# Kernel tuning notes

Measured on AMD Instinct MI355X. Metric: run time of the kernel, lower is better.

The kernel has to match this reference:

```python
import jax, jax.numpy as jnp
import numpy as np

ENC_DIM = 256
DEC_DIM = 256
INT_DIM = 256


def setup_inputs() -> dict:
    key = jax.random.key(0)
    k1, k2, k3, k4, k5 = jax.random.split(key, 5)
    B, T = 64, 2048
    encoder_states = jax.random.normal(k1, (B, T, ENC_DIM), dtype=jnp.float32)
    decoder_state = jax.random.normal(k2, (B, DEC_DIM), dtype=jnp.float32)
    s1 = 1.0 / np.sqrt(ENC_DIM)
    s2 = 1.0 / np.sqrt(DEC_DIM)
    s3 = 1.0 / np.sqrt(INT_DIM)
    w1 = jax.random.uniform(k3, (INT_DIM, ENC_DIM), jnp.float32, -s1, s1)
    w2 = jax.random.uniform(k4, (INT_DIM, DEC_DIM), jnp.float32, -s2, s2)
    v = jax.random.uniform(k5, (1, INT_DIM), jnp.float32, -s3, s3)
    return {"encoder_states": encoder_states, "decoder_state": decoder_state,
            "w1": w1, "w2": w2, "v": v}


def reference(encoder_states, decoder_state, w1, w2, v):
    # scores: v @ tanh(W1 e_t + W2 d) for all t at once
    enc_proj = jnp.einsum('bte,ie->bti', encoder_states, w1)      # [B,T,I]
    dec_proj = jnp.einsum('bd,id->bi', decoder_state, w2)          # [B,I]
    scores = jnp.einsum('bti,oi->bt', jnp.tanh(enc_proj + dec_proj[:, None, :]), v)  # [B,T]
    attention_probs = jax.nn.softmax(scores, axis=1)[:, :, None]   # [B,T,1]
    final_context_vec = jnp.sum(attention_probs * encoder_states, axis=1)  # [B,E]
    return final_context_vec, attention_probs
```

## Files before the change

kernel.cpp:

```cpp
#include <hip/hip_runtime.h>
#include <hip/hip_bf16.h>
#include <math.h>

#define Bq 64
#define Tq 2048
#define Eq 256
#define Dq 256
#define Iq 256

using short8  = __attribute__((ext_vector_type(8))) short;
using floatx4 = __attribute__((ext_vector_type(4))) float;

__device__ __forceinline__ float fast_tanh(float x) {
    float e = __expf(2.0f * x);
    return fmaf(-2.0f, __builtin_amdgcn_rcpf(e + 1.0f), 1.0f);
}

__device__ __forceinline__ ushort f2bf(float x) {
    union { __hip_bfloat16 h; ushort u; } c;
    c.h = __float2bfloat16(x);
    return c.u;
}

__global__ __launch_bounds__(256) void prep_kernel(
    const float* __restrict__ w1, ushort* __restrict__ w1sw,
    const float* __restrict__ dec, const float* __restrict__ w2,
    float* __restrict__ dproj)
{
    if (blockIdx.x < 32) {
        const int kc = blockIdx.x;
        const int i  = threadIdx.x;
        const float* src = w1 + i * Eq + kc * 8;
        float4 f0 = *(const float4*)src;
        float4 f1 = *(const float4*)(src + 4);
        ushort u[8] = { f2bf(f0.x), f2bf(f0.y), f2bf(f0.z), f2bf(f0.w),
                        f2bf(f1.x), f2bf(f1.y), f2bf(f1.z), f2bf(f1.w) };
        *(short8*)&w1sw[(kc * 256 + i) * 8] = *(short8*)u;
    } else {
        const int b = blockIdx.x - 32;
        const int i = threadIdx.x;
        __shared__ float dls[Dq];
        dls[i] = dec[b * Dq + i];
        __syncthreads();
        const float* w2r = w2 + i * Dq;
        float acc = 0.f;
        #pragma unroll 8
        for (int d = 0; d < Dq; d += 4) {
            float4 wv = *(const float4*)&w2r[d];
            float4 dv = *(const float4*)&dls[d];
            acc += wv.x * dv.x + wv.y * dv.y + wv.z * dv.z + wv.w * dv.w;
        }
        dproj[b * Iq + i] = acc;
    }
}

__global__ __launch_bounds__(256, 3) void scores_ctx_kernel(
    const float*  __restrict__ enc,
    const ushort* __restrict__ w1sw,
    const float*  __restrict__ v,
    const float*  __restrict__ dproj,
    float* __restrict__ escore,
    float* __restrict__ ctxp,
    float* __restrict__ denomp)
{
    const int b   = blockIdx.y;
    const int bx  = blockIdx.x;
    const int t0  = bx * 64;
    const int tid = threadIdx.x;
    const int w   = tid >> 6;
    const int l   = tid & 63;
    const int l15 = l & 15;
    const int lq  = l >> 4;

    __shared__ alignas(16) ushort As[2][64 * 72];
    __shared__ float swred[4 * 64];
    __shared__ float redf[4 * 256];

    float vv[4], dd[4];
    #pragma unroll
    for (int ni = 0; ni < 4; ++ni) {
        const int i = w * 64 + ni * 16 + l15;
        vv[ni] = v[i];
        dd[ni] = dproj[b * Iq + i];
    }

    floatx4 acc[4][4];
    #pragma unroll
    for (int mi = 0; mi < 4; ++mi)
        #pragma unroll
        for (int ni = 0; ni < 4; ++ni)
            acc[mi][ni] = (floatx4)0.f;

    const float* encB = enc + ((size_t)b * Tq + t0) * Eq;
    const int srow = tid >> 4;
    const int sc4  = (tid & 15) * 4;

    #define LOADC(kt, st)                                                     \
        _Pragma("unroll")                                                     \
        for (int r = 0; r < 4; ++r)                                           \
            st[r] = *(const float4*)&encB[(srow + 16 * r) * Eq + (kt) * 64 + sc4];
    #define CVTW(st, buf)                                                     \
        _Pragma("unroll")                                                     \
        for (int r = 0; r < 4; ++r) {                                         \
            ushort4 u;                                                        \
            u.x = f2bf(st[r].x); u.y = f2bf(st[r].y);                         \
            u.z = f2bf(st[r].z); u.w = f2bf(st[r].w);                         \
            *(ushort4*)&As[buf][(srow + 16 * r) * 72 + sc4] = u;              \
        }
    #define BARRIER()                                                         \
        asm volatile("s_waitcnt lgkmcnt(0)" ::: "memory");                    \
        __builtin_amdgcn_s_barrier();                                         \
        __builtin_amdgcn_sched_barrier(0);

    const ushort* vb = w1sw + (w * 64 + l15) * 8 + lq * 2048;

    #define KSTEP(k, cur, LOADNEXT, CVTPREV)                                  \
    {                                                                         \
        short8 bfv[2][4];                                                     \
        _Pragma("unroll")                                                     \
        for (int ks = 0; ks < 2; ++ks)                                        \
            _Pragma("unroll")                                                 \
            for (int ni = 0; ni < 4; ++ni)                                    \
                bfv[ks][ni] = *(const short8*)(vb + ((k) * 8 + ks * 4) * 2048 \
                                               + ni * 128);                   \
        LOADNEXT                                                              \
        _Pragma("unroll")                                                     \
        for (int ks = 0; ks < 2; ++ks) {                                      \
            const int kloc = ks * 32 + lq * 8;                                \
            short8 af[4];                                                     \
            _Pragma("unroll")                                                 \
            for (int mi = 0; mi < 4; ++mi)                                    \
                af[mi] = *(const short8*)&As[cur][(mi * 16 + l15) * 72 + kloc];\
            __builtin_amdgcn_s_setprio(1);                                    \
            _Pragma("unroll")                                                 \
            for (int mi = 0; mi < 4; ++mi)                                    \
                _Pragma("unroll")                                             \
                for (int ni = 0; ni < 4; ++ni)                                \
                    acc[mi][ni] = __builtin_amdgcn_mfma_f32_16x16x32_bf16(    \
                        af[mi], bfv[ks][ni], acc[mi][ni], 0, 0, 0);           \
            __builtin_amdgcn_s_setprio(0);                                    \
        }                                                                     \
        CVTPREV                                                               \
    }

    float4 s0[4], s1[4];
    LOADC(0, s0);
    LOADC(1, s1);
    CVTW(s0, 0);
    BARRIER();

    KSTEP(0, 0, LOADC(2, s0);, CVTW(s1, 1); BARRIER();)
    KSTEP(1, 1, LOADC(3, s1);, CVTW(s0, 0); BARRIER();)
    KSTEP(2, 0, ;,             CVTW(s1, 1); BARRIER();)
    KSTEP(3, 1, ;,             ;)

    #undef KSTEP
    #undef LOADC
    #undef CVTW

    float part[4][4];
    #pragma unroll
    for (int mi = 0; mi < 4; ++mi)
        #pragma unroll
        for (int r = 0; r < 4; ++r) part[mi][r] = 0.f;

    #pragma unroll
    for (int ni = 0; ni < 4; ++ni) {
        const float vi = vv[ni];
        const float dp = dd[ni];
        #pragma unroll
        for (int mi = 0; mi < 4; ++mi)
            #pragma unroll
            for (int r = 0; r < 4; ++r)
                part[mi][r] += vi * fast_tanh(acc[mi][ni][r] + dp);
    }

    #pragma unroll
    for (int mi = 0; mi < 4; ++mi)
        #pragma unroll
        for (int r = 0; r < 4; ++r) {
            float x = part[mi][r];
            x += __shfl_xor(x, 1); x += __shfl_xor(x, 2);
            x += __shfl_xor(x, 4); x += __shfl_xor(x, 8);
            part[mi][r] = x;
        }
    if (l15 == 0) {
        #pragma unroll
        for (int mi = 0; mi < 4; ++mi)
            #pragma unroll
            for (int r = 0; r < 4; ++r)
                swred[w * 64 + mi * 16 + lq * 4 + r] = part[mi][r];
    }
    __syncthreads();

    float s = swred[l] + swred[64 + l] + swred[128 + l] + swred[192 + l];
    const float es = __expf(s);
    if (w == 0) {
        escore[(size_t)b * Tq + t0 + l] = es;
        float tot = es;
        tot += __shfl_xor(tot, 1);  tot += __shfl_xor(tot, 2);
        tot += __shfl_xor(tot, 4);  tot += __shfl_xor(tot, 8);
        tot += __shfl_xor(tot, 16); tot += __shfl_xor(tot, 32);
        if (l == 0) denomp[bx * Bq + b] = tot;
    }

    const int el = l * 4;
    float4 a = {0.f, 0.f, 0.f, 0.f};
    #pragma unroll 8
    for (int tt = 0; tt < 16; ++tt) {
        const int t = w * 16 + tt;
        const float pt = __shfl(es, t);
        float4 ev = *(const float4*)&encB[t * Eq + el];
        a.x += pt * ev.x; a.y += pt * ev.y; a.z += pt * ev.z; a.w += pt * ev.w;
    }
    *(float4*)&redf[w * 256 + el] = a;
    __syncthreads();
    if (w == 0) {
        float4 a0 = *(const float4*)&redf[0 * 256 + el];
        float4 a1 = *(const float4*)&redf[1 * 256 + el];
        float4 a2 = *(const float4*)&redf[2 * 256 + el];
        float4 a3 = *(const float4*)&redf[3 * 256 + el];
        float4 o;
        o.x = a0.x + a1.x + a2.x + a3.x;
        o.y = a0.y + a1.y + a2.y + a3.y;
        o.z = a0.z + a1.z + a2.z + a3.z;
        o.w = a0.w + a1.w + a2.w + a3.w;
        *(float4*)&ctxp[((size_t)bx * Bq + b) * Eq + el] = o;
    }
}

__global__ __launch_bounds__(256) void finalize_kernel(
    const float* __restrict__ ctxp, const float* __restrict__ denomp,
    float* __restrict__ probs, float* __restrict__ ctx)
{
    const int b   = blockIdx.x;
    const int tid = threadIdx.x;

    float d = denomp[(tid & 31) * Bq + b];
    d += __shfl_xor(d, 1);  d += __shfl_xor(d, 2);  d += __shfl_xor(d, 4);
    d += __shfl_xor(d, 8);  d += __shfl_xor(d, 16);
    const float inv = 1.0f / d;

    float* prow = probs + (size_t)b * Tq + tid * 8;
    float4 p0 = *(const float4*)(prow + 0);
    float4 p1 = *(const float4*)(prow + 4);
    p0.x *= inv; p0.y *= inv; p0.z *= inv; p0.w *= inv;
    p1.x *= inv; p1.y *= inv; p1.z *= inv; p1.w *= inv;
    *(float4*)(prow + 0) = p0;
    *(float4*)(prow + 4) = p1;

    float s = 0.f;
    #pragma unroll 8
    for (int c = 0; c < 32; ++c)
        s += ctxp[((size_t)c * Bq + b) * Eq + tid];
    ctx[b * Eq + tid] = s * inv;
}

extern "C" void kernel_launch(void* const* d_in, const int* in_sizes, int n_in,
                              void* d_out, int out_size, void* d_ws, size_t ws_size,
                              hipStream_t stream) {
    const float* enc = (const float*)d_in[0];
    const float* dec = (const float*)d_in[1];
    const float* w1  = (const float*)d_in[2];
    const float* w2  = (const float*)d_in[3];
    const float* v   = (const float*)d_in[4];

    float* out   = (float*)d_out;
    float* ctx   = out;
    float* probs = out + Bq * Eq;

    char* ws = (char*)d_ws;
    float*  ctxp   = (float*)ws;
    float*  denomp = (float*)(ws + (32*Bq*Eq)*4);
    float*  dproj  = (float*)(ws + (32*Bq*Eq)*4 + 32*Bq*4);
    ushort* w1sw   = (ushort*)(ws + (32*Bq*Eq)*4 + 32*Bq*4 + Bq*Iq*4);

    prep_kernel<<<dim3(96), dim3(256), 0, stream>>>(w1, w1sw, dec, w2, dproj);
    scores_ctx_kernel<<<dim3(Tq / 64, Bq), dim3(256), 0, stream>>>(
        enc, w1sw, v, dproj, probs, ctxp, denomp);
    finalize_kernel<<<dim3(Bq), dim3(256), 0, stream>>>(ctxp, denomp, probs, ctx);
}
```

Before: 218.3 us.

## Process two T-tiles per block and prefetch next tile's loads during the first epilogue

Each block now handles two consecutive 64-row time tiles instead of one, halving the grid. The first k-chunks of the second tile are loaded from global memory during the last MFMA steps of the first tile, so that load latency overlaps the first tile's tanh/softmax/context epilogue. This amortizes per-block setup (v, dproj loads) and hides the pipeline fill. In exchange the grid has fewer blocks (16x64), which may reduce occupancy and tail balance, and registers holding the prefetched tile stay live across the epilogue.

```diff
diff --git a/kernel.cpp b/kernel.cpp
--- a/kernel.cpp
+++ b/kernel.cpp
@@ -54,6 +54,91 @@
     }
 }
 
+__device__ __forceinline__ void tile_epilogue(
+    floatx4 (&acc)[4][4], const float (&vv)[4], const float (&dd)[4],
+    float* swred, float* redf, const float* eb,
+    float* __restrict__ escore, float* __restrict__ ctxp,
+    float* __restrict__ denomp,
+    int b, int bxx, int w, int l, int l15, int lq)
+{
+    float part[4][4];
+    #pragma unroll
+    for (int mi = 0; mi < 4; ++mi)
+        #pragma unroll
+        for (int r = 0; r < 4; ++r) part[mi][r] = 0.f;
+
+    #pragma unroll
+    for (int ni = 0; ni < 4; ++ni) {
+        const float vi = vv[ni];
+        const float dp = dd[ni];
+        #pragma unroll
+        for (int mi = 0; mi < 4; ++mi)
+            #pragma unroll
+            for (int r = 0; r < 4; ++r)
+                part[mi][r] += vi * fast_tanh(acc[mi][ni][r] + dp);
+    }
+
+    #pragma unroll
+    for (int mi = 0; mi < 4; ++mi)
+        #pragma unroll
+        for (int r = 0; r < 4; ++r) {
+            float x = part[mi][r];
+            x += __shfl_xor(x, 1); x += __shfl_xor(x, 2);
+            x += __shfl_xor(x, 4); x += __shfl_xor(x, 8);
+            part[mi][r] = x;
+        }
+    if (l15 == 0) {
+        #pragma unroll
+        for (int mi = 0; mi < 4; ++mi)
+            #pragma unroll
+            for (int r = 0; r < 4; ++r)
+                swred[w * 64 + mi * 16 + lq * 4 + r] = part[mi][r];
+    }
+    asm volatile("s_waitcnt lgkmcnt(0)" ::: "memory");
+    __builtin_amdgcn_s_barrier();
+    __builtin_amdgcn_sched_barrier(0);
+
+    float s = swred[l] + swred[64 + l] + swred[128 + l] + swred[192 + l];
+    const float es = __expf(s);
+    if (w == 0) {
+        escore[(size_t)b * Tq + bxx * 64 + l] = es;
+        float tot = es;
+        tot += __shfl_xor(tot, 1);  tot += __shfl_xor(tot, 2);
+        tot += __shfl_xor(tot, 4);  tot += __shfl_xor(tot, 8);
+        tot += __shfl_xor(tot, 16); tot += __shfl_xor(tot, 32);
+        if (l == 0) denomp[bxx * Bq + b] = tot;
+    }
+
+    const int el = l * 4;
+    float4 a = {0.f, 0.f, 0.f, 0.f};
+    #pragma unroll 8
+    for (int tt = 0; tt < 16; ++tt) {
+        const int t = w * 16 + tt;
+        const float pt = __shfl(es, t);
+        float4 ev = *(const float4*)&eb[t * Eq + el];
+        a.x += pt * ev.x; a.y += pt * ev.y; a.z += pt * ev.z; a.w += pt * ev.w;
+    }
+    *(float4*)&redf[w * 256 + el] = a;
+    asm volatile("s_waitcnt lgkmcnt(0)" ::: "memory");
+    __builtin_amdgcn_s_barrier();
+    __builtin_amdgcn_sched_barrier(0);
+    if (w == 0) {
+        float4 a0 = *(const float4*)&redf[0 * 256 + el];
+        float4 a1 = *(const float4*)&redf[1 * 256 + el];
+        float4 a2 = *(const float4*)&redf[2 * 256 + el];
+        float4 a3 = *(const float4*)&redf[3 * 256 + el];
+        float4 o;
+        o.x = a0.x + a1.x + a2.x + a3.x;
+        o.y = a0.y + a1.y + a2.y + a3.y;
+        o.z = a0.z + a1.z + a2.z + a3.z;
+        o.w = a0.w + a1.w + a2.w + a3.w;
+        *(float4*)&ctxp[((size_t)bxx * Bq + b) * Eq + el] = o;
+    }
+    asm volatile("s_waitcnt lgkmcnt(0)" ::: "memory");
+    __builtin_amdgcn_s_barrier();
+    __builtin_amdgcn_sched_barrier(0);
+}
+
 __global__ __launch_bounds__(256, 3) void scores_ctx_kernel(
     const float*  __restrict__ enc,
     const ushort* __restrict__ w1sw,
@@ -64,8 +149,7 @@
     float* __restrict__ denomp)
 {
     const int b   = blockIdx.y;
-    const int bx  = blockIdx.x;
-    const int t0  = bx * 64;
+    const int bx0 = blockIdx.x * 2;
     const int tid = threadIdx.x;
     const int w   = tid >> 6;
     const int l   = tid & 63;
@@ -85,20 +169,16 @@
     }
 
     floatx4 acc[4][4];
-    #pragma unroll
-    for (int mi = 0; mi < 4; ++mi)
-        #pragma unroll
-        for (int ni = 0; ni < 4; ++ni)
-            acc[mi][ni] = (floatx4)0.f;
-
-    const float* encB = enc + ((size_t)b * Tq + t0) * Eq;
+
+    const float* encT0 = enc + ((size_t)b * Tq + bx0 * 64) * Eq;
+    const float* encT1 = encT0 + (size_t)64 * Eq;
     const int srow = tid >> 4;
     const int sc4  = (tid & 15) * 4;
 
-    #define LOADC(kt, st)                                                     \
+    #define LOADC(eb, kt, st)                                                 \
         _Pragma("unroll")                                                     \
         for (int r = 0; r < 4; ++r)                                           \
-            st[r] = *(const float4*)&encB[(srow + 16 * r) * Eq + (kt) * 64 + sc4];
+            st[r] = *(const float4*)&eb[(srow + 16 * r) * Eq + (kt) * 64 + sc4];
     #define CVTW(st, buf)                                                     \
         _Pragma("unroll")                                                     \
         for (int r = 0; r < 4; ++r) {                                         \
@@ -144,89 +224,47 @@
     }
 
     float4 s0[4], s1[4];
-    LOADC(0, s0);
-    LOADC(1, s1);
+
+    LOADC(encT0, 0, s0);
+    LOADC(encT0, 1, s1);
     CVTW(s0, 0);
     BARRIER();
 
-    KSTEP(0, 0, LOADC(2, s0);, CVTW(s1, 1); BARRIER();)
-    KSTEP(1, 1, LOADC(3, s1);, CVTW(s0, 0); BARRIER();)
-    KSTEP(2, 0, ;,             CVTW(s1, 1); BARRIER();)
-    KSTEP(3, 1, ;,             ;)
+    #pragma unroll
+    for (int mi = 0; mi < 4; ++mi)
+        #pragma unroll
+        for (int ni = 0; ni < 4; ++ni)
+            acc[mi][ni] = (floatx4)0.f;
+
+    KSTEP(0, 0, LOADC(encT0, 2, s0);, CVTW(s1, 1); BARRIER();)
+    KSTEP(1, 1, LOADC(encT0, 3, s1);, CVTW(s0, 0); BARRIER();)
+    KSTEP(2, 0, LOADC(encT1, 0, s0);, CVTW(s1, 1); BARRIER();)
+    KSTEP(3, 1, LOADC(encT1, 1, s1);, ;)
+
+    tile_epilogue(acc, vv, dd, swred, redf, encT0,
+                  escore, ctxp, denomp, b, bx0, w, l, l15, lq);
+
+    CVTW(s0, 0);
+    BARRIER();
+
+    #pragma unroll
+    for (int mi = 0; mi < 4; ++mi)
+        #pragma unroll
+        for (int ni = 0; ni < 4; ++ni)
+            acc[mi][ni] = (floatx4)0.f;
+
+    KSTEP(0, 0, LOADC(encT1, 2, s0);, CVTW(s1, 1); BARRIER();)
+    KSTEP(1, 1, LOADC(encT1, 3, s1);, CVTW(s0, 0); BARRIER();)
+    KSTEP(2, 0, ;,                    CVTW(s1, 1); BARRIER();)
+    KSTEP(3, 1, ;,                    ;)
+
+    tile_epilogue(acc, vv, dd, swred, redf, encT1,
+                  escore, ctxp, denomp, b, bx0 + 1, w, l, l15, lq);
 
     #undef KSTEP
     #undef LOADC
     #undef CVTW
-
-    float part[4][4];
-    #pragma unroll
-    for (int mi = 0; mi < 4; ++mi)
-        #pragma unroll
-        for (int r = 0; r < 4; ++r) part[mi][r] = 0.f;
-
-    #pragma unroll
-    for (int ni = 0; ni < 4; ++ni) {
-        const float vi = vv[ni];
-        const float dp = dd[ni];
-        #pragma unroll
-        for (int mi = 0; mi < 4; ++mi)
-            #pragma unroll
-            for (int r = 0; r < 4; ++r)
-                part[mi][r] += vi * fast_tanh(acc[mi][ni][r] + dp);
-    }
-
-    #pragma unroll
-    for (int mi = 0; mi < 4; ++mi)
-        #pragma unroll
-        for (int r = 0; r < 4; ++r) {
-            float x = part[mi][r];
-            x += __shfl_xor(x, 1); x += __shfl_xor(x, 2);
-            x += __shfl_xor(x, 4); x += __shfl_xor(x, 8);
-            part[mi][r] = x;
-        }
-    if (l15 == 0) {
-        #pragma unroll
-        for (int mi = 0; mi < 4; ++mi)
-            #pragma unroll
-            for (int r = 0; r < 4; ++r)
-                swred[w * 64 + mi * 16 + lq * 4 + r] = part[mi][r];
-    }
-    __syncthreads();
-
-    float s = swred[l] + swred[64 + l] + swred[128 + l] + swred[192 + l];
-    const float es = __expf(s);
-    if (w == 0) {
-        escore[(size_t)b * Tq + t0 + l] = es;
-        float tot = es;
-        tot += __shfl_xor(tot, 1);  tot += __shfl_xor(tot, 2);
-        tot += __shfl_xor(tot, 4);  tot += __shfl_xor(tot, 8);
-        tot += __shfl_xor(tot, 16); tot += __shfl_xor(tot, 32);
-        if (l == 0) denomp[bx * Bq + b] = tot;
-    }
-
-    const int el = l * 4;
-    float4 a = {0.f, 0.f, 0.f, 0.f};
-    #pragma unroll 8
-    for (int tt = 0; tt < 16; ++tt) {
-        const int t = w * 16 + tt;
-        const float pt = __shfl(es, t);
-        float4 ev = *(const float4*)&encB[t * Eq + el];
-        a.x += pt * ev.x; a.y += pt * ev.y; a.z += pt * ev.z; a.w += pt * ev.w;
-    }
-    *(float4*)&redf[w * 256 + el] = a;
-    __syncthreads();
-    if (w == 0) {
-        float4 a0 = *(const float4*)&redf[0 * 256 + el];
-        float4 a1 = *(const float4*)&redf[1 * 256 + el];
-        float4 a2 = *(const float4*)&redf[2 * 256 + el];
-        float4 a3 = *(const float4*)&redf[3 * 256 + el];
-        float4 o;
-        o.x = a0.x + a1.x + a2.x + a3.x;
-        o.y = a0.y + a1.y + a2.y + a3.y;
-        o.z = a0.z + a1.z + a2.z + a3.z;
-        o.w = a0.w + a1.w + a2.w + a3.w;
-        *(float4*)&ctxp[((size_t)bx * Bq + b) * Eq + el] = o;
-    }
+    #undef BARRIER
 }
 
 __global__ __launch_bounds__(256) void finalize_kernel(
@@ -276,7 +314,7 @@
     ushort* w1sw   = (ushort*)(ws + (32*Bq*Eq)*4 + 32*Bq*4 + Bq*Iq*4);
 
     prep_kernel<<<dim3(96), dim3(256), 0, stream>>>(w1, w1sw, dec, w2, dproj);
-    scores_ctx_kernel<<<dim3(Tq / 64, Bq), dim3(256), 0, stream>>>(
+    scores_ctx_kernel<<<dim3(Tq / 128, Bq), dim3(256), 0, stream>>>(
         enc, w1sw, v, dproj, probs, ctxp, denomp);
     finalize_kernel<<<dim3(Bq), dim3(256), 0, stream>>>(ctxp, denomp, probs, ctx);
 }
```

New measurement: 270.4 us. 23.9% more time.
